# Optimization experiments

Measured on AMD Instinct MI355X. Metric: run time of the kernel, lower is better.

Reference implementation:

```python
import jax, jax.numpy as jnp
import numpy as np

NEG_INF = -1e9  # matches torch masked_fill value of -1000000000.0


def setup_inputs() -> dict:
    key = jax.random.key(0)
    kq, kk, kv, km = jax.random.split(key, 4)
    B, H, L, D = 4, 16, 1024, 64
    query = jax.random.normal(kq, (B, H, L, D), dtype=jnp.float32)
    k_ = jax.random.normal(kk, (B, H, L, D), dtype=jnp.float32)
    value = jax.random.normal(kv, (B, H, L, D), dtype=jnp.float32)
    mask = jax.random.randint(km, (B, 1, L, L), 0, 2, dtype=jnp.int32)
    return {"query": query, "key": k_, "value": value, "mask": mask}


def reference(query, key, value, mask):
    # scores: [B, H, Lq, Lk]
    d = query.shape[-1]
    scores = jnp.einsum("bhqd,bhkd->bhqk", query, key) / jnp.sqrt(jnp.float32(d))
    masked = mask == 0  # broadcast [B,1,Lq,Lk] over heads
    scores = jnp.where(masked, jnp.float32(NEG_INF), scores)
    p_attn = jax.nn.softmax(scores, axis=-1)
    p_attn = jnp.where(masked, jnp.float32(0.0), p_attn)
    out = jnp.einsum("bhqk,bhkd->bhqd", p_attn, value)
    return out, p_attn
```

## Files before the change

### kernel.cpp

```cpp
#include <hip/hip_runtime.h>
#include <math.h>

typedef __attribute__((ext_vector_type(8))) short short8;
typedef __attribute__((ext_vector_type(4))) float f32x4;

#define NB 4
#define NH 16
#define SL 1024
#define DH 64
#define BQ 64
#define WQ 16
#define KTL 64
#define NT 256
#define NKT (SL / KTL)

#define TILE_SH (KTL * DH)
#define HEAD_SH ((size_t)NKT * TILE_SH)
#define BLOB_SH ((size_t)NB * NH * HEAD_SH)
#define BMROW   (SL / 32)

#define QSCALE 0.18033688011111543f
#define NEGB  -1.5e9f

#if __has_builtin(__builtin_amdgcn_exp2f)
#define EXP2F(x) __builtin_amdgcn_exp2f(x)
#else
#define EXP2F(x) exp2f(x)
#endif

__device__ __forceinline__ unsigned short bf_rne(float x) {
    unsigned int u = __float_as_uint(x);
    u += 0x7fffu + ((u >> 16) & 1u);
    return (unsigned short)(u >> 16);
}
__device__ __forceinline__ void bf_split(float x, unsigned short& h, unsigned short& l) {
    unsigned int u = __float_as_uint(x);
    h = (unsigned short)(u >> 16);
    float r = x - __uint_as_float(u & 0xffff0000u);
    l = bf_rne(r);
}

__device__ __forceinline__ unsigned pk16(float a, float b) {
    _Float16 ha = (_Float16)a, hb = (_Float16)b;
    unsigned short ua = __builtin_bit_cast(unsigned short, ha);
    unsigned short ub = __builtin_bit_cast(unsigned short, hb);
    return (unsigned)ua | ((unsigned)ub << 16);
}
__device__ __forceinline__ void upk16(unsigned u, float& a, float& b) {
    _Float16 ha = __builtin_bit_cast(_Float16, (unsigned short)(u & 0xffffu));
    _Float16 hb = __builtin_bit_cast(_Float16, (unsigned short)(u >> 16));
    a = (float)ha;
    b = (float)hb;
}

typedef const __attribute__((address_space(1))) unsigned int guint_t;
typedef __attribute__((address_space(3))) unsigned int luint_t;
__device__ __forceinline__ void gload_lds16(const void* g, void* l) {
    __builtin_amdgcn_global_load_lds((guint_t*)g, (luint_t*)l, 16, 0, 0);
}

#define MFMA(a, b, c) __builtin_amdgcn_mfma_f32_16x16x32_bf16(a, b, c, 0, 0, 0)

#define WAITVM(N) do { asm volatile("s_waitcnt vmcnt(" #N ")" ::: "memory"); \
                       __builtin_amdgcn_sched_barrier(0); } while (0)
#define BAR() do { __builtin_amdgcn_sched_barrier(0); __builtin_amdgcn_s_barrier(); \
                   __builtin_amdgcn_sched_barrier(0); } while (0)
#define SCHED_FENCE() __builtin_amdgcn_sched_barrier(0)

__global__ __launch_bounds__(NT, 4) void prep_mask(
    const int* __restrict__ M, unsigned* __restrict__ bm)
{
    const size_t total = (size_t)NB * SL * SL;
    const int l = threadIdx.x & 63;
    for (size_t i = (size_t)blockIdx.x * NT + threadIdx.x; i < total;
         i += (size_t)gridDim.x * NT) {
        int v = M[i];
        unsigned long long b = __ballot(v != 0);
        if (l == 0)       bm[i >> 5] = (unsigned)b;
        else if (l == 32) bm[i >> 5] = (unsigned)(b >> 32);
    }
}

__global__ __launch_bounds__(NT, 2) void prep_split(
    const float* __restrict__ K, const float* __restrict__ V,
    unsigned short* __restrict__ kb, unsigned short* __restrict__ vb)
{
    __shared__ float sVs[KTL][DH + 4];

    const int t = threadIdx.x;
    const int kt = blockIdx.x, h = blockIdx.y, b = blockIdx.z;
    const size_t goff = (size_t)(b * NH + h) * SL * DH + (size_t)kt * KTL * DH;
    const size_t tks = (size_t)(b * NH + h) * HEAD_SH + (size_t)kt * TILE_SH;

    #pragma unroll
    for (int u = 0; u < 2; ++u) {
        int idx = u * NT + t;
        int kr = idx >> 3, c8 = idx & 7;
        const float* src = K + goff + kr * DH + c8 * 8;
        float4 a = *(const float4*)src;
        float4 bb = *(const float4*)(src + 4);
        float vals[8] = {a.x, a.y, a.z, a.w, bb.x, bb.y, bb.z, bb.w};
        unsigned int pk[4];
        #pragma unroll
        for (int j = 0; j < 4; ++j)
            pk[j] = (unsigned int)bf_rne(vals[2 * j]) |
                    ((unsigned int)bf_rne(vals[2 * j + 1]) << 16);
        int dsw = (c8 * 8) ^ ((kr & 7) << 3);
        *(uint4*)&kb[tks + kr * DH + dsw] = make_uint4(pk[0], pk[1], pk[2], pk[3]);
    }

    #pragma unroll
    for (int u = 0; u < 4; ++u) {
        int i = u * NT + t;
        float4 v = *(const float4*)(V + goff + (size_t)i * 4);
        *(float4*)&sVs[i >> 4][(i & 15) * 4] = v;
    }
    __syncthreads();
    #pragma unroll
    for (int u = 0; u < 2; ++u) {
        int idx = u * NT + t;
        int d = idx & 63, k8 = idx >> 6;
        float vals[8];
        #pragma unroll
        for (int j = 0; j < 8; ++j) vals[j] = sVs[k8 * 8 + j][d];
        unsigned int pk[4];
        #pragma unroll
        for (int j = 0; j < 4; ++j)
            pk[j] = (unsigned int)bf_rne(vals[2 * j]) |
                    ((unsigned int)bf_rne(vals[2 * j + 1]) << 16);
        int ksw = (k8 * 8) ^ ((d & 7) << 3);
        *(uint4*)&vb[tks + d * KTL + ksw] = make_uint4(pk[0], pk[1], pk[2], pk[3]);
    }
}

__global__ __launch_bounds__(NT, 2) void attn_one(
    const float* __restrict__ Q, const unsigned* __restrict__ bm,
    const unsigned short* __restrict__ kb, const unsigned short* __restrict__ vb,
    float* __restrict__ O, float* __restrict__ P)
{
    __shared__ unsigned short sS[2][TILE_SH];
    __shared__ unsigned short sPh[4][WQ][KTL];

    const int t = threadIdx.x;
    const int l = t & 63;
    const int w = __builtin_amdgcn_readfirstlane(t >> 6);
    const int lg = l >> 4, lr = l & 15;

    const int flat = blockIdx.x + (blockIdx.y << 4) + (blockIdx.z << 8);
    const int nid = (flat & 7) * 128 + (flat >> 3);
    const int qt = nid & 15;
    const int hh_ = (nid >> 4) & 15;
    const int b = nid >> 8;
    const int qb = qt * BQ + w * WQ;

    const size_t hoff = (size_t)(b * NH + hh_) * SL * DH;
    const size_t headsh = (size_t)(b * NH + hh_) * HEAD_SH;
    const unsigned short* kbh = kb + headsh;
    const unsigned short* vbh = vb + headsh;
    const unsigned* bmRow = bm + ((size_t)b * SL + qb + lr) * BMROW;
    float* Pw = P + ((size_t)(b * NH + hh_) * SL + qb) * SL;
    float* Ow = O + hoff + (size_t)qb * DH;

    short8 qf[2];
    {
        const float* src0 = Q + hoff + (size_t)(qb + lr) * DH + lg * 8;
        #pragma unroll
        for (int ds = 0; ds < 2; ++ds) {
            const float* src = src0 + ds * 32;
            float4 a = *(const float4*)src;
            float4 bb = *(const float4*)(src + 4);
            float vals[8] = {a.x, a.y, a.z, a.w, bb.x, bb.y, bb.z, bb.w};
            #pragma unroll
            for (int j = 0; j < 8; ++j)
                qf[ds][j] = (short)bf_rne(vals[j] * QSCALE);
        }
    }

    auto stage = [&](unsigned short* lds, const unsigned short* gt) {
        #pragma unroll
        for (int u = 0; u < 2; ++u) {
            const int c = w * 2 + u;
            gload_lds16((const char*)gt + c * 1024 + l * 16, (char*)lds + c * 1024);
        }
    };

    const f32x4 zero = {0.f, 0.f, 0.f, 0.f};
    unsigned su[NKT][8];
    float psum = 0.f;
    uint2 bmv, bmn;

    stage(sS[0], kbh);
    bmv = *(const uint2*)&bmRow[0];

    #pragma unroll
    for (int kt = 0; kt < NKT; ++kt) {
        WAITVM(0);
        BAR();
        if (kt + 1 < NKT) {
            stage(sS[(kt + 1) & 1], kbh + (size_t)(kt + 1) * TILE_SH);
            bmn = *(const uint2*)&bmRow[2 * (kt + 1)];
        }
        SCHED_FENCE();

        f32x4 acc[4];
        #pragma unroll
        for (int st = 0; st < 4; ++st) {
            const int krow = st * 16 + lr;
            const int sw = (krow & 7) << 3;
            short8 a0 = *(const short8*)&sS[kt & 1][krow * DH + ((lg * 8) ^ sw)];
            short8 a1 = *(const short8*)&sS[kt & 1][krow * DH + ((32 + lg * 8) ^ sw)];
            f32x4 c = MFMA(a0, qf[0], zero);
            acc[st] = MFMA(a1, qf[1], c);
        }

        float ts = 0.f;
        #pragma unroll
        for (int st = 0; st < 4; ++st) {
            const unsigned bmd = (st & 2) ? bmv.y : bmv.x;
            float s[4];
            #pragma unroll
            for (int j = 0; j < 4; ++j) {
                unsigned bit = (bmd >> ((st & 1) * 16 + lg * 4 + j)) & 1u;
                s[j] = acc[st][j] + (bit ? 0.f : NEGB);
                ts += EXP2F(s[j]);
            }
            su[kt][st * 2 + 0] = pk16(s[0], s[1]);
            su[kt][st * 2 + 1] = pk16(s[2], s[3]);
        }
        psum += ts;
        bmv = bmn;
    }

    float sum = psum;
    sum += __shfl_xor(sum, 16);
    sum += __shfl_xor(sum, 32);
    sum = fmaxf(sum, 1e-35f);
    const float m2 = __log2f(sum);

    WAITVM(0);
    BAR();
    f32x4 oacc[4];
    #pragma unroll
    for (int mt = 0; mt < 4; ++mt) oacc[mt] = zero;

    stage(sS[0], vbh);

    #pragma unroll
    for (int kt = 0; kt < NKT; ++kt) {
        const int k0 = kt * KTL;
        if (kt == 0) { WAITVM(0); } else { WAITVM(4); }
        BAR();
        if (kt + 1 < NKT)
            stage(sS[(kt + 1) & 1], vbh + (size_t)(kt + 1) * TILE_SH);
        SCHED_FENCE();

        #pragma unroll
        for (int st = 0; st < 4; ++st) {
            float s[4];
            upk16(su[kt][st * 2 + 0], s[0], s[1]);
            upk16(su[kt][st * 2 + 1], s[2], s[3]);
            float p[4];
            #pragma unroll
            for (int j = 0; j < 4; ++j) p[j] = EXP2F(s[j] - m2);
            f32x4 pv4 = {p[0], p[1], p[2], p[3]};
            __builtin_nontemporal_store(
                pv4, (f32x4*)(Pw + (size_t)lr * SL + (k0 + st * 16 + lg * 4)));
            int col = (st * 16 + lg * 4) ^ ((lr & 7) << 3);
            uint2 uh;
            uh.x = (unsigned int)bf_rne(p[0]) | ((unsigned int)bf_rne(p[1]) << 16);
            uh.y = (unsigned int)bf_rne(p[2]) | ((unsigned int)bf_rne(p[3]) << 16);
            *(uint2*)&sPh[w][lr][col] = uh;
        }

        short8 pb0 = *(const short8*)&sPh[w][lr][(lg * 8) ^ ((lr & 7) << 3)];
        short8 pb1 = *(const short8*)&sPh[w][lr][(32 + lg * 8) ^ ((lr & 7) << 3)];
        #pragma unroll
        for (int mt = 0; mt < 4; ++mt) {
            const int d = mt * 16 + lr;
            const int sw = (d & 7) << 3;
            short8 v0 = *(const short8*)&sS[kt & 1][d * KTL + ((lg * 8) ^ sw)];
            short8 v1 = *(const short8*)&sS[kt & 1][d * KTL + ((32 + lg * 8) ^ sw)];
            oacc[mt] = MFMA(v0, pb0, oacc[mt]);
            oacc[mt] = MFMA(v1, pb1, oacc[mt]);
        }
    }

    #pragma unroll
    for (int mt = 0; mt < 4; ++mt) {
        __builtin_nontemporal_store(
            oacc[mt], (f32x4*)(Ow + (size_t)lr * DH + mt * 16 + lg * 4));
    }
}

__global__ __launch_bounds__(NT, 2) void attn_fallback(
    const float* __restrict__ Q, const float* __restrict__ K,
    const float* __restrict__ V, const int* __restrict__ M,
    float* __restrict__ O, float* __restrict__ P)
{
    __shared__ unsigned short sKhi[64][DH];
    __shared__ unsigned short sKlo[64][DH];
    __shared__ unsigned short sVhi[DH][64];
    __shared__ unsigned short sVlo[DH][64];
    __shared__ unsigned short sPhi[4][WQ][64];
    __shared__ unsigned short sPlo[4][WQ][64];

    const int t = threadIdx.x;
    const int l = t & 63;
    const int w = t >> 6;
    const int lg = l >> 4;
    const int lr = l & 15;

    const int hh_ = blockIdx.y, b = blockIdx.z;
    const int qb = blockIdx.x * BQ + w * WQ;

    const size_t hoff = (size_t)(b * NH + hh_) * SL * DH;
    const float* Kh = K + hoff;
    const float* Vh = V + hoff;
    const int*   Mw = M + ((size_t)b * SL + qb) * SL;
    float*       Pw = P + ((size_t)(b * NH + hh_) * SL + qb) * SL;
    float*       Ow = O + hoff + (size_t)qb * DH;

    short8 qhi[2], qlo[2];
    {
        const float* src0 = Q + hoff + (size_t)(qb + lr) * DH + lg * 8;
        #pragma unroll
        for (int ds = 0; ds < 2; ++ds) {
            const float* src = src0 + ds * 32;
            float4 a = *(const float4*)src;
            float4 bb = *(const float4*)(src + 4);
            float vals[8] = {a.x, a.y, a.z, a.w, bb.x, bb.y, bb.z, bb.w};
            #pragma unroll
            for (int j = 0; j < 8; ++j) {
                unsigned short hv, lv;
                bf_split(vals[j] * 0.125f, hv, lv);
                qhi[ds][j] = (short)hv;
                qlo[ds][j] = (short)lv;
            }
        }
    }

    auto stageK = [&](int k0) {
        #pragma unroll
        for (int u = 0; u < 2; ++u) {
            int idx = u * NT + t;
            int kr = idx >> 3;
            int dc = (idx & 7) * 8;
            const float* src = Kh + (size_t)(k0 + kr) * DH + dc;
            float4 a = *(const float4*)src;
            float4 bb = *(const float4*)(src + 4);
            float vals[8] = {a.x, a.y, a.z, a.w, bb.x, bb.y, bb.z, bb.w};
            unsigned int ph[4], pl[4];
            #pragma unroll
            for (int j = 0; j < 4; ++j) {
                unsigned short h0, l0, h1, l1;
                bf_split(vals[2 * j], h0, l0);
                bf_split(vals[2 * j + 1], h1, l1);
                ph[j] = (unsigned int)h0 | ((unsigned int)h1 << 16);
                pl[j] = (unsigned int)l0 | ((unsigned int)l1 << 16);
            }
            int dsw = dc ^ ((kr & 7) << 3);
            *(uint4*)&sKhi[kr][dsw] = make_uint4(ph[0], ph[1], ph[2], ph[3]);
            *(uint4*)&sKlo[kr][dsw] = make_uint4(pl[0], pl[1], pl[2], pl[3]);
        }
    };

    float m = -INFINITY, sum = 0.f;
    for (int kt = 0; kt < 16; ++kt) {
        const int k0 = kt * 64;
        __syncthreads();
        stageK(k0);
        __syncthreads();
        f32x4 acc[4];
        #pragma unroll
        for (int st = 0; st < 4; ++st) {
            const int krow = st * 16 + lr;
            const int sw = (krow & 7) << 3;
            f32x4 c = {0.f, 0.f, 0.f, 0.f};
            #pragma unroll
            for (int ds = 0; ds < 2; ++ds) {
                int dc = (ds * 32 + lg * 8) ^ sw;
                short8 ah = *(const short8*)&sKhi[krow][dc];
                short8 al = *(const short8*)&sKlo[krow][dc];
                c = MFMA(ah, qhi[ds], c);
                c = MFMA(ah, qlo[ds], c);
                c = MFMA(al, qhi[ds], c);
            }
            acc[st] = c;
        }
        float s[16];
        #pragma unroll
        for (int st = 0; st < 4; ++st) {
            const int4 mv = *(const int4*)(Mw + (size_t)lr * SL + k0 + st * 16 + lg * 4);
            s[st * 4 + 0] = mv.x ? acc[st][0] : -1e9f;
            s[st * 4 + 1] = mv.y ? acc[st][1] : -1e9f;
            s[st * 4 + 2] = mv.z ? acc[st][2] : -1e9f;
            s[st * 4 + 3] = mv.w ? acc[st][3] : -1e9f;
        }
        float tmax = s[0];
        #pragma unroll
        for (int j = 1; j < 16; ++j) tmax = fmaxf(tmax, s[j]);
        tmax = fmaxf(tmax, __shfl_xor(tmax, 16));
        tmax = fmaxf(tmax, __shfl_xor(tmax, 32));
        const float mn = fmaxf(m, tmax);
        float ts = 0.f;
        #pragma unroll
        for (int j = 0; j < 16; ++j) ts += __expf(s[j] - mn);
        ts += __shfl_xor(ts, 16);
        ts += __shfl_xor(ts, 32);
        sum = sum * __expf(m - mn) + ts;
        m = mn;
    }
    const float inv = 1.f / sum;

    f32x4 oacc[4];
    #pragma unroll
    for (int mt = 0; mt < 4; ++mt) oacc[mt] = (f32x4){0.f, 0.f, 0.f, 0.f};

    for (int kt = 0; kt < 16; ++kt) {
        const int k0 = kt * 64;
        __syncthreads();
        stageK(k0);
        {
            int d0 = (t & 15) * 4;
            int kl0 = (t >> 4) * 4;
            float4 r[4];
            #pragma unroll
            for (int i = 0; i < 4; ++i)
                r[i] = *(const float4*)(Vh + (size_t)(k0 + kl0 + i) * DH + d0);
            const float* rp = (const float*)r;
            #pragma unroll
            for (int j = 0; j < 4; ++j) {
                unsigned short hv[4], lv[4];
                #pragma unroll
                for (int i = 0; i < 4; ++i) bf_split(rp[i * 4 + j], hv[i], lv[i]);
                int d = d0 + j;
                int csw = kl0 ^ ((d & 7) << 3);
                uint2 uh, ul;
                uh.x = (unsigned int)hv[0] | ((unsigned int)hv[1] << 16);
                uh.y = (unsigned int)hv[2] | ((unsigned int)hv[3] << 16);
                ul.x = (unsigned int)lv[0] | ((unsigned int)lv[1] << 16);
                ul.y = (unsigned int)lv[2] | ((unsigned int)lv[3] << 16);
                *(uint2*)&sVhi[d][csw] = uh;
                *(uint2*)&sVlo[d][csw] = ul;
            }
        }
        __syncthreads();

        #pragma unroll
        for (int st = 0; st < 4; ++st) {
            const int krow = st * 16 + lr;
            const int sw = (krow & 7) << 3;
            f32x4 c = {0.f, 0.f, 0.f, 0.f};
            #pragma unroll
            for (int ds = 0; ds < 2; ++ds) {
                int dc = (ds * 32 + lg * 8) ^ sw;
                short8 ah = *(const short8*)&sKhi[krow][dc];
                short8 al = *(const short8*)&sKlo[krow][dc];
                c = MFMA(ah, qhi[ds], c);
                c = MFMA(ah, qlo[ds], c);
                c = MFMA(al, qhi[ds], c);
            }
            const int4 mv = *(const int4*)(Mw + (size_t)lr * SL + k0 + st * 16 + lg * 4);
            float p0 = mv.x ? __expf(c[0] - m) * inv : 0.f;
            float p1 = mv.y ? __expf(c[1] - m) * inv : 0.f;
            float p2 = mv.z ? __expf(c[2] - m) * inv : 0.f;
            float p3 = mv.w ? __expf(c[3] - m) * inv : 0.f;
            *(float4*)(Pw + (size_t)lr * SL + (k0 + st * 16 + lg * 4)) =
                make_float4(p0, p1, p2, p3);
            unsigned short hv[4], lv[4];
            bf_split(p0, hv[0], lv[0]);
            bf_split(p1, hv[1], lv[1]);
            bf_split(p2, hv[2], lv[2]);
            bf_split(p3, hv[3], lv[3]);
            int col = (st * 16 + lg * 4) ^ ((lr & 7) << 3);
            uint2 uh, ul;
            uh.x = (unsigned int)hv[0] | ((unsigned int)hv[1] << 16);
            uh.y = (unsigned int)hv[2] | ((unsigned int)hv[3] << 16);
            ul.x = (unsigned int)lv[0] | ((unsigned int)lv[1] << 16);
            ul.y = (unsigned int)lv[2] | ((unsigned int)lv[3] << 16);
            *(uint2*)&sPhi[w][lr][col] = uh;
            *(uint2*)&sPlo[w][lr][col] = ul;
        }

        short8 pbh[2], pbl[2];
        #pragma unroll
        for (int ks = 0; ks < 2; ++ks) {
            int col = (ks * 32 + lg * 8) ^ ((lr & 7) << 3);
            pbh[ks] = *(const short8*)&sPhi[w][lr][col];
            pbl[ks] = *(const short8*)&sPlo[w][lr][col];
        }
        #pragma unroll
        for (int mt = 0; mt < 4; ++mt) {
            const int d = mt * 16 + lr;
            const int swd = (d & 7) << 3;
            #pragma unroll
            for (int ks = 0; ks < 2; ++ks) {
                int col = (ks * 32 + lg * 8) ^ swd;
                short8 vh = *(const short8*)&sVhi[d][col];
                short8 vl = *(const short8*)&sVlo[d][col];
                oacc[mt] = MFMA(vh, pbh[ks], oacc[mt]);
                oacc[mt] = MFMA(vh, pbl[ks], oacc[mt]);
                oacc[mt] = MFMA(vl, pbh[ks], oacc[mt]);
            }
        }
    }

    #pragma unroll
    for (int mt = 0; mt < 4; ++mt) {
        float4 o = make_float4(oacc[mt][0], oacc[mt][1], oacc[mt][2], oacc[mt][3]);
        *(float4*)(Ow + (size_t)lr * DH + mt * 16 + lg * 4) = o;
    }
}

extern "C" void kernel_launch(void* const* d_in, const int* in_sizes, int n_in,
                              void* d_out, int out_size, void* d_ws, size_t ws_size,
                              hipStream_t stream) {
    const float* Q = (const float*)d_in[0];
    const float* K = (const float*)d_in[1];
    const float* V = (const float*)d_in[2];
    const int*   M = (const int*)d_in[3];
    float* O = (float*)d_out;
    float* P = O + (size_t)NB * NH * SL * DH;

    const size_t bm_dw = (size_t)NB * SL * BMROW;
    const size_t need = bm_dw * 4 + 2 * BLOB_SH * 2;
    if (ws_size >= need) {
        unsigned* bmp = (unsigned*)d_ws;
        unsigned short* kbp = (unsigned short*)(bmp + bm_dw);
        unsigned short* vbp = kbp + BLOB_SH;
        hipLaunchKernelGGL(prep_mask, dim3(1024, 1, 1), dim3(NT, 1, 1), 0, stream, M, bmp);
        hipLaunchKernelGGL(prep_split, dim3(NKT, NH, NB), dim3(NT, 1, 1), 0, stream,
                           K, V, kbp, vbp);
        hipLaunchKernelGGL(attn_one, dim3(SL / BQ, NH, NB), dim3(NT, 1, 1), 0, stream,
                           Q, bmp, kbp, vbp, O, P);
    } else {
        hipLaunchKernelGGL(attn_fallback, dim3(SL / BQ, NH, NB), dim3(NT, 1, 1), 0, stream,
                           Q, K, V, M, O, P);
    }
}
```

Measured before the change: 142.7 us.

## Defer P writes to an epilogue staged through LDS for coalesced row stores

Instead of writing each probability tile to global memory inside the PV loop with scattered 16-byte stores, the kernel keeps bf16-packed probabilities in registers. After the loop it stages them through a new LDS buffer and writes full 1 KB contiguous row segments per wavefront. This is meant to improve store coalescing and take global stores out of the MFMA loop. In exchange, P is now rounded to bf16 before being written as fp32, which reduces output precision. It also adds LDS use (about 33 KB), which may lower occupancy, and the V prefetch wait is tightened to vmcnt(0).

Result: faster. 127.6 us (-10.6%).

```diff
diff --git a/kernel.cpp b/kernel.cpp
--- a/kernel.cpp
+++ b/kernel.cpp
@@ -140,6 +140,7 @@
 {
     __shared__ unsigned short sS[2][TILE_SH];
     __shared__ unsigned short sPh[4][WQ][KTL];
+    __shared__ unsigned short sPb[BQ][264];
 
     const int t = threadIdx.x;
     const int l = t & 63;
@@ -158,7 +159,7 @@
     const unsigned short* kbh = kb + headsh;
     const unsigned short* vbh = vb + headsh;
     const unsigned* bmRow = bm + ((size_t)b * SL + qb + lr) * BMROW;
-    float* Pw = P + ((size_t)(b * NH + hh_) * SL + qb) * SL;
+    float* Pblk = P + (((size_t)(b * NH + hh_) * SL) + (size_t)qt * BQ) * SL;
     float* Ow = O + hoff + (size_t)qb * DH;
 
     short8 qf[2];
@@ -247,8 +248,7 @@
 
     #pragma unroll
     for (int kt = 0; kt < NKT; ++kt) {
-        const int k0 = kt * KTL;
-        if (kt == 0) { WAITVM(0); } else { WAITVM(4); }
+        WAITVM(0);
         BAR();
         if (kt + 1 < NKT)
             stage(sS[(kt + 1) & 1], vbh + (size_t)(kt + 1) * TILE_SH);
@@ -262,14 +262,12 @@
             float p[4];
             #pragma unroll
             for (int j = 0; j < 4; ++j) p[j] = EXP2F(s[j] - m2);
-            f32x4 pv4 = {p[0], p[1], p[2], p[3]};
-            __builtin_nontemporal_store(
-                pv4, (f32x4*)(Pw + (size_t)lr * SL + (k0 + st * 16 + lg * 4)));
+            unsigned u0 = (unsigned)bf_rne(p[0]) | ((unsigned)bf_rne(p[1]) << 16);
+            unsigned u1 = (unsigned)bf_rne(p[2]) | ((unsigned)bf_rne(p[3]) << 16);
+            su[kt][st * 2 + 0] = u0;
+            su[kt][st * 2 + 1] = u1;
             int col = (st * 16 + lg * 4) ^ ((lr & 7) << 3);
-            uint2 uh;
-            uh.x = (unsigned int)bf_rne(p[0]) | ((unsigned int)bf_rne(p[1]) << 16);
-            uh.y = (unsigned int)bf_rne(p[2]) | ((unsigned int)bf_rne(p[3]) << 16);
-            *(uint2*)&sPh[w][lr][col] = uh;
+            *(uint2*)&sPh[w][lr][col] = make_uint2(u0, u1);
         }
 
         short8 pb0 = *(const short8*)&sPh[w][lr][(lg * 8) ^ ((lr & 7) << 3)];
@@ -289,6 +287,35 @@
     for (int mt = 0; mt < 4; ++mt) {
         __builtin_nontemporal_store(
             oacc[mt], (f32x4*)(Ow + (size_t)lr * DH + mt * 16 + lg * 4));
+    }
+
+    BAR();
+    #pragma unroll
+    for (int g = 0; g < 4; ++g) {
+        #pragma unroll
+        for (int kk = 0; kk < 4; ++kk) {
+            const int kt = g * 4 + kk;
+            #pragma unroll
+            for (int st = 0; st < 4; ++st) {
+                const int c = kk * 64 + st * 16 + lg * 4;
+                *(uint2*)&sPb[w * WQ + lr][c] =
+                    make_uint2(su[kt][st * 2 + 0], su[kt][st * 2 + 1]);
+            }
+        }
+        BAR();
+        #pragma unroll
+        for (int it = 0; it < 16; ++it) {
+            const int row = it * 4 + w;
+            const uint2 u = *(const uint2*)&sPb[row][l * 4];
+            f32x4 pv;
+            pv[0] = __uint_as_float(u.x << 16);
+            pv[1] = __uint_as_float(u.x & 0xffff0000u);
+            pv[2] = __uint_as_float(u.y << 16);
+            pv[3] = __uint_as_float(u.y & 0xffff0000u);
+            __builtin_nontemporal_store(
+                pv, (f32x4*)(Pblk + (size_t)row * SL + g * 256 + l * 4));
+        }
+        BAR();
     }
 }
 
```
